# Performance work log

Measured on AMD Instinct MI355X. Metric: run time of the kernel, lower is better.

Reference implementation:

```python
import jax, jax.numpy as jnp
import numpy as np

N, K, C = 32768, 64, 256
PAIR, HID, BINS, CLIP = 32, 64, 16, 32
LN_EPS = 1e-5


def setup_inputs() -> dict:
    key = jax.random.key(0)
    ks = jax.random.split(key, 12)
    inp = {
        "features": jax.random.normal(ks[0], (N, C), jnp.float32),
        "resi": jnp.arange(N, dtype=jnp.int32),
        "chain": jax.random.randint(ks[1], (N,), 0, 4, jnp.int32),
        "batch": jax.random.randint(ks[2], (N,), 0, 8, jnp.int32),
        "neighbours": jax.random.randint(ks[3], (N, K), 0, N, jnp.int32),
        # learned params
        "W_left": jax.random.normal(ks[4], (C, PAIR), jnp.float32) / np.sqrt(C),
        "W_right": jax.random.normal(ks[5], (C, PAIR), jnp.float32) / np.sqrt(C),
        "W_pos": jax.random.normal(ks[6], (2 * CLIP + 1, PAIR), jnp.float32) * 0.1,
        "ln_scale": jnp.ones((PAIR,), jnp.float32),
        "ln_bias": jnp.zeros((PAIR,), jnp.float32),
        "W1": jax.random.normal(ks[7], (PAIR, HID), jnp.float32) / np.sqrt(PAIR),
        "b1": jnp.zeros((HID,), jnp.float32),
        "W2": jax.random.normal(ks[8], (HID, BINS), jnp.float32) / np.sqrt(HID),
        "b2": jnp.zeros((BINS,), jnp.float32),
    }
    return inp


def reference(features, resi, chain, batch, neighbours,
              W_left, W_right, W_pos, ln_scale, ln_bias, W1, b1, W2, b2):
    # left/right 32-dim codes, pairwise combine via neighbour gather: [N,K,32]
    left = features @ W_left
    right = features @ W_right
    dcode = left[:, None, :] + right[neighbours]

    # relative sequence position one-hot (65 classes) -> Linear(32, bias=False).
    # one_hot @ W_pos == row-gather of W_pos; masked to same chain & batch.
    rel = jnp.clip(resi[neighbours] - resi[:, None], -CLIP, CLIP) + CLIP  # [N,K]
    same = (chain[neighbours] == chain[:, None]) & (batch[neighbours] == batch[:, None])
    dcode = dcode + jnp.where(same[..., None], W_pos[rel], 0.0)

    # LayerNorm over last axis (scale + offset)
    mu = dcode.mean(-1, keepdims=True)
    var = jnp.mean(jnp.square(dcode - mu), -1, keepdims=True)
    dcode = (dcode - mu) * jax.lax.rsqrt(var + LN_EPS) * ln_scale + ln_bias

    # 2-layer GELU MLP -> 16 bins
    h = jax.nn.gelu(dcode @ W1 + b1)
    logits = h @ W2 + b2
    log_p = jax.nn.log_softmax(logits, axis=-1)

    # softmax-weighted expected distance over bin centers of [0, 22) A
    step = 22.0 / BINS
    bin_centers = (jnp.arange(BINS, dtype=jnp.float32) + 0.5) * step
    dmap = (jnp.exp(log_p) * bin_centers).sum(axis=-1)  # [N,K]
    return log_p, dmap
```

## Files before the change

### kernel.cpp

```cpp
#include <hip/hip_runtime.h>
#include <stdint.h>

#define N_RES 32768
#define KNEI  64
#define CFEAT 256
#define PAIRD 32
#define HIDD  64
#define NBINS 16
#define CLIPV 32
#define NGROUPS (N_RES * KNEI / 16)

typedef __attribute__((ext_vector_type(8))) short  short8;
typedef __attribute__((ext_vector_type(4))) float  float4_t;

union U8 { uint32_t u[4]; short8 s8; };

__device__ __forceinline__ uint32_t f2bf(float a, float b) {
    uint32_t ua = __float_as_uint(a);
    uint32_t ub = __float_as_uint(b);
    ua += 0x7fffu + ((ua >> 16) & 1u);
    ub += 0x7fffu + ((ub >> 16) & 1u);
    return (ua >> 16) | (ub & 0xffff0000u);
}

__device__ __forceinline__ float fastrcp(float x) { return __builtin_amdgcn_rcpf(x); }

__device__ __forceinline__ float gelu_tanh(float x) {
    float x2 = x * x;
    float inner = 0.7978845608028654f * x * (1.0f + 0.044715f * x2);
    float e = __expf(2.0f * inner);
    float th = 1.0f - 2.0f * fastrcp(e + 1.0f);
    return 0.5f * x * (1.0f + th);
}

__global__ __launch_bounds__(256) void proj_kernel(
    const float* __restrict__ feat, const float* __restrict__ Wl,
    const float* __restrict__ Wr, float* __restrict__ left,
    float* __restrict__ right)
{
    __shared__ __align__(16) float Wc[CFEAT * 64];
    const int tid = threadIdx.x;
    for (int idx = tid; idx < CFEAT * 32; idx += 256) {
        int i = idx >> 5, o = idx & 31;
        Wc[i * 64 + o]      = Wl[idx];
        Wc[i * 64 + 32 + o] = Wr[idx];
    }
    __syncthreads();

    const int cb   = (tid & 7) * 8;
    const int row0 = blockIdx.x * 128 + (tid >> 3) * 4;

    float acc[4][8];
#pragma unroll
    for (int r = 0; r < 4; ++r)
#pragma unroll
        for (int j = 0; j < 8; ++j) acc[r][j] = 0.f;

    for (int i = 0; i < CFEAT; i += 4) {
        float4_t f[4];
#pragma unroll
        for (int r = 0; r < 4; ++r)
            f[r] = *(const float4_t*)(feat + (size_t)(row0 + r) * CFEAT + i);
#pragma unroll
        for (int s = 0; s < 4; ++s) {
            float4_t wa = *(const float4_t*)(Wc + (i + s) * 64 + cb);
            float4_t wb = *(const float4_t*)(Wc + (i + s) * 64 + cb + 4);
#pragma unroll
            for (int r = 0; r < 4; ++r) {
                float fv = f[r][s];
#pragma unroll
                for (int j = 0; j < 4; ++j) {
                    acc[r][j]     += fv * wa[j];
                    acc[r][4 + j] += fv * wb[j];
                }
            }
        }
    }
#pragma unroll
    for (int r = 0; r < 4; ++r) {
        float* dst = (cb < 32) ? (left  + (size_t)(row0 + r) * 32 + cb)
                               : (right + (size_t)(row0 + r) * 32 + (cb - 32));
        float4_t v0 = {acc[r][0], acc[r][1], acc[r][2], acc[r][3]};
        float4_t v1 = {acc[r][4], acc[r][5], acc[r][6], acc[r][7]};
        *(float4_t*)dst       = v0;
        *(float4_t*)(dst + 4) = v1;
    }
}

__global__ __launch_bounds__(256) void pair_kernel(
    const float* __restrict__ left, const float* __restrict__ right,
    const int* __restrict__ resi, const int* __restrict__ chain,
    const int* __restrict__ batch, const int* __restrict__ nbr,
    const float* __restrict__ wpos, const float* __restrict__ lnS,
    const float* __restrict__ lnB, const float* __restrict__ W1,
    const float* __restrict__ b1, const float* __restrict__ W2,
    const float* __restrict__ b2, float* __restrict__ out_logp,
    float* __restrict__ out_dmap)
{
    __shared__ __align__(16) unsigned char Hbuf[4][16 * 144];

    const int tid    = threadIdx.x;
    const int lane   = tid & 63;
    const int wlocal = tid >> 6;
    const int q      = lane >> 4;
    const int c      = lane & 15;

    short8 w1a[4];
#pragma unroll
    for (int t = 0; t < 4; ++t) {
        U8 tmp;
#pragma unroll
        for (int v = 0; v < 4; ++v) {
            float a0 = W1[(q * 8 + 2 * v)     * HIDD + 16 * t + c];
            float a1 = W1[(q * 8 + 2 * v + 1) * HIDD + 16 * t + c];
            tmp.u[v] = f2bf(a0, a1);
        }
        w1a[t] = tmp.s8;
    }
    short8 w2a[2];
#pragma unroll
    for (int kt = 0; kt < 2; ++kt) {
        U8 tmp;
#pragma unroll
        for (int v = 0; v < 4; ++v) {
            float a0 = W2[(kt * 32 + q * 8 + 2 * v)     * NBINS + c];
            float a1 = W2[(kt * 32 + q * 8 + 2 * v + 1) * NBINS + c];
            tmp.u[v] = f2bf(a0, a1);
        }
        w2a[kt] = tmp.s8;
    }
    float4_t b1f[4];
#pragma unroll
    for (int t = 0; t < 4; ++t)
        b1f[t] = *(const float4_t*)(b1 + 16 * t + 4 * q);
    const float4_t b2f  = *(const float4_t*)(b2 + 4 * q);
    const float4_t lnS0 = *(const float4_t*)(lnS + 8 * q);
    const float4_t lnS1 = *(const float4_t*)(lnS + 8 * q + 4);
    const float4_t lnB0 = *(const float4_t*)(lnB + 8 * q);
    const float4_t lnB1 = *(const float4_t*)(lnB + 8 * q + 4);
    const float4_t zero4 = {0.f, 0.f, 0.f, 0.f};

    const int wglobal = (blockIdx.x * 256 + tid) >> 6;
    const int nwaves  = (gridDim.x * 256) >> 6;

    for (int g = wglobal; g < NGROUPS; g += nwaves) {
        const int pbase = g * 16;
        const int n = pbase >> 6;
        const int p = pbase + c;
        const int nb = nbr[p];
        const int rn = resi[n], cn = chain[n], bn = batch[n];
        int rel = resi[nb] - rn;
        rel = min(max(rel, -CLIPV), CLIPV) + CLIPV;
        const float msk = ((chain[nb] == cn) && (batch[nb] == bn)) ? 1.0f : 0.0f;

        const float* lptr = left  + (size_t)n  * PAIRD + 8 * q;
        const float* rptr = right + (size_t)nb * PAIRD + 8 * q;
        const float* pptr = wpos  + (size_t)rel * PAIRD + 8 * q;
        float4_t l0 = *(const float4_t*)lptr,       l1 = *(const float4_t*)(lptr + 4);
        float4_t r0 = *(const float4_t*)rptr,       r1 = *(const float4_t*)(rptr + 4);
        float4_t p0 = *(const float4_t*)pptr,       p1 = *(const float4_t*)(pptr + 4);
        float d[8];
#pragma unroll
        for (int j = 0; j < 4; ++j) {
            d[j]     = l0[j] + r0[j] + msk * p0[j];
            d[4 + j] = l1[j] + r1[j] + msk * p1[j];
        }

        float s1 = 0.f, s2 = 0.f;
#pragma unroll
        for (int j = 0; j < 8; ++j) { s1 += d[j]; s2 += d[j] * d[j]; }
        s1 += __shfl_xor(s1, 16, 64);  s1 += __shfl_xor(s1, 32, 64);
        s2 += __shfl_xor(s2, 16, 64);  s2 += __shfl_xor(s2, 32, 64);
        const float mu   = s1 * (1.0f / 32.0f);
        const float var  = s2 * (1.0f / 32.0f) - mu * mu;
        const float rstd = __builtin_amdgcn_rsqf(var + 1e-5f);

        U8 dpack;
#pragma unroll
        for (int v = 0; v < 4; ++v) {
            int j0 = 2 * v, j1 = 2 * v + 1;
            float sA = (j0 < 4) ? lnS0[j0 & 3] : lnS1[j0 & 3];
            float bA = (j0 < 4) ? lnB0[j0 & 3] : lnB1[j0 & 3];
            float sB = (j1 < 4) ? lnS0[j1 & 3] : lnS1[j1 & 3];
            float bB = (j1 < 4) ? lnB0[j1 & 3] : lnB1[j1 & 3];
            float nA = (d[j0] - mu) * rstd * sA + bA;
            float nB = (d[j1] - mu) * rstd * sB + bB;
            dpack.u[v] = f2bf(nA, nB);
        }
        const short8 dfrag = dpack.s8;

        float4_t hacc[4];
#pragma unroll
        for (int t = 0; t < 4; ++t)
            hacc[t] = __builtin_amdgcn_mfma_f32_16x16x32_bf16(w1a[t], dfrag, zero4, 0, 0, 0);

        unsigned char* hb = &Hbuf[wlocal][0] + c * 144;
#pragma unroll
        for (int t = 0; t < 4; ++t) {
            float g0 = gelu_tanh(hacc[t][0] + b1f[t][0]);
            float g1 = gelu_tanh(hacc[t][1] + b1f[t][1]);
            float g2 = gelu_tanh(hacc[t][2] + b1f[t][2]);
            float g3 = gelu_tanh(hacc[t][3] + b1f[t][3]);
            uint2 w; w.x = f2bf(g0, g1); w.y = f2bf(g2, g3);
            *(uint2*)(hb + 32 * t + 8 * q) = w;
        }
        __asm__ __volatile__("s_waitcnt lgkmcnt(0)" ::: "memory");
        const short8 hf0 = *(const short8*)(hb + 16 * q);
        const short8 hf1 = *(const short8*)(hb + 64 + 16 * q);

        float4_t lacc;
        lacc = __builtin_amdgcn_mfma_f32_16x16x32_bf16(w2a[0], hf0, zero4, 0, 0, 0);
        lacc = __builtin_amdgcn_mfma_f32_16x16x32_bf16(w2a[1], hf1, lacc,  0, 0, 0);

        float l[4];
#pragma unroll
        for (int r = 0; r < 4; ++r) l[r] = lacc[r] + b2f[r];

        float mx = fmaxf(fmaxf(l[0], l[1]), fmaxf(l[2], l[3]));
        mx = fmaxf(mx, __shfl_xor(mx, 16, 64));
        mx = fmaxf(mx, __shfl_xor(mx, 32, 64));
        float e[4];
#pragma unroll
        for (int r = 0; r < 4; ++r) e[r] = __expf(l[r] - mx);
        float ssum = (e[0] + e[1]) + (e[2] + e[3]);
        ssum += __shfl_xor(ssum, 16, 64);
        ssum += __shfl_xor(ssum, 32, 64);
        const float lse = __logf(ssum);

        float4_t lp = {l[0] - mx - lse, l[1] - mx - lse,
                       l[2] - mx - lse, l[3] - mx - lse};
        *(float4_t*)(out_logp + (size_t)p * NBINS + 4 * q) = lp;

        const float step  = 22.0f / NBINS;
        const float cbase = (4 * q + 0.5f) * step;
        float dpart = e[0] * cbase + e[1] * (cbase + step)
                    + e[2] * (cbase + 2 * step) + e[3] * (cbase + 3 * step);
        dpart += __shfl_xor(dpart, 16, 64);
        dpart += __shfl_xor(dpart, 32, 64);
        if (q == 0) out_dmap[p] = dpart * fastrcp(ssum);
    }
}

extern "C" void kernel_launch(void* const* d_in, const int* in_sizes, int n_in,
                              void* d_out, int out_size, void* d_ws, size_t ws_size,
                              hipStream_t stream) {
    const float* features = (const float*)d_in[0];
    const int*   resi     = (const int*)d_in[1];
    const int*   chain    = (const int*)d_in[2];
    const int*   batch    = (const int*)d_in[3];
    const int*   nbr      = (const int*)d_in[4];
    const float* W_left   = (const float*)d_in[5];
    const float* W_right  = (const float*)d_in[6];
    const float* W_pos    = (const float*)d_in[7];
    const float* ln_scale = (const float*)d_in[8];
    const float* ln_bias  = (const float*)d_in[9];
    const float* W1       = (const float*)d_in[10];
    const float* b1       = (const float*)d_in[11];
    const float* W2       = (const float*)d_in[12];
    const float* b2       = (const float*)d_in[13];

    float* left  = (float*)d_ws;
    float* right = left + (size_t)N_RES * PAIRD;

    float* out_logp = (float*)d_out;
    float* out_dmap = out_logp + (size_t)N_RES * KNEI * NBINS;

    proj_kernel<<<N_RES / 128, 256, 0, stream>>>(features, W_left, W_right, left, right);
    pair_kernel<<<2048, 256, 0, stream>>>(left, right, resi, chain, batch, nbr,
                                          W_pos, ln_scale, ln_bias, W1, b1, W2, b2,
                                          out_logp, out_dmap);
}
```

Measured before the change: 336.0 us.

## Fold LayerNorm affine into W1, drop softmax max, pack metadata, cheapen math

Folds the LayerNorm scale and bias into W1 and a precomputed b1 held in shared memory. The folded biases are fed as the MFMA accumulator input, and the softmax skips the max-subtraction and uses exp2/log2 intrinsics. GELU is rewritten around exp2 with folded constants, and bf16 packing uses an add-and-v_perm rounding instead of round-to-nearest-even. The projection kernel also writes a packed resi/chain/batch int4 array, so the pair kernel makes one gather per residue instead of three. The projection uses smaller row tiles, the pair kernel gains an occupancy hint, and an explicit LDS waitcnt is removed. Dropping the max subtraction risks overflow if logits get large, and the changed rounding shifts numerics slightly.

New measurement: 311.5 us. 7.3% less time.

```diff
diff --git a/kernel.cpp b/kernel.cpp
--- a/kernel.cpp
+++ b/kernel.cpp
@@ -15,71 +15,80 @@
 
 union U8 { uint32_t u[4]; short8 s8; };
 
-__device__ __forceinline__ uint32_t f2bf(float a, float b) {
-    uint32_t ua = __float_as_uint(a);
-    uint32_t ub = __float_as_uint(b);
-    ua += 0x7fffu + ((ua >> 16) & 1u);
-    ub += 0x7fffu + ((ub >> 16) & 1u);
-    return (ua >> 16) | (ub & 0xffff0000u);
+__device__ __forceinline__ uint32_t pkbf(float a, float b) {
+    uint32_t ua = __float_as_uint(a) + 0x8000u;
+    uint32_t ub = __float_as_uint(b) + 0x8000u;
+    uint32_t d;
+    const uint32_t sel = 0x07060302u;
+    asm("v_perm_b32 %0, %1, %2, %3" : "=v"(d) : "v"(ub), "v"(ua), "s"(sel));
+    return d;
 }
 
 __device__ __forceinline__ float fastrcp(float x) { return __builtin_amdgcn_rcpf(x); }
+__device__ __forceinline__ float fexp2(float x)   { return __builtin_amdgcn_exp2f(x); }
+__device__ __forceinline__ float flog2(float x)   { return __builtin_amdgcn_logf(x); }
 
 __device__ __forceinline__ float gelu_tanh(float x) {
+    const float k1 = 2.3022082f;
+    const float k2 = 0.1029432f;
     float x2 = x * x;
-    float inner = 0.7978845608028654f * x * (1.0f + 0.044715f * x2);
-    float e = __expf(2.0f * inner);
-    float th = 1.0f - 2.0f * fastrcp(e + 1.0f);
-    return 0.5f * x * (1.0f + th);
+    float t  = __builtin_fmaf(k2, x2, k1);
+    float e  = fexp2(x * t);
+    float th = __builtin_fmaf(-2.0f, fastrcp(e + 1.0f), 1.0f);
+    float hx = 0.5f * x;
+    return __builtin_fmaf(hx, th, hx);
 }
 
 __global__ __launch_bounds__(256) void proj_kernel(
     const float* __restrict__ feat, const float* __restrict__ Wl,
-    const float* __restrict__ Wr, float* __restrict__ left,
-    float* __restrict__ right)
+    const float* __restrict__ Wr, const int* __restrict__ resi,
+    const int* __restrict__ chain, const int* __restrict__ batch,
+    float* __restrict__ left, float* __restrict__ right,
+    int4* __restrict__ meta)
 {
     __shared__ __align__(16) float Wc[CFEAT * 64];
     const int tid = threadIdx.x;
     for (int idx = tid; idx < CFEAT * 32; idx += 256) {
-        int i = idx >> 5, o = idx & 31;
-        Wc[i * 64 + o]      = Wl[idx];
-        Wc[i * 64 + 32 + o] = Wr[idx];
+        int k = idx >> 5, o = idx & 31;
+        Wc[k * 64 + o]      = Wl[idx];
+        Wc[k * 64 + 32 + o] = Wr[idx];
+    }
+    const int row_base = blockIdx.x * 64;
+    if (meta != nullptr && tid < 64) {
+        int r = row_base + tid;
+        meta[r] = make_int4(resi[r], chain[r], batch[r], 0);
     }
     __syncthreads();
 
-    const int cb   = (tid & 7) * 8;
-    const int row0 = blockIdx.x * 128 + (tid >> 3) * 4;
-
-    float acc[4][8];
-#pragma unroll
-    for (int r = 0; r < 4; ++r)
+    const int cb = (tid & 7) * 8;
+    const int r0 = row_base + (tid >> 3) * 2;
+
+    float acc[2][8];
+#pragma unroll
+    for (int r = 0; r < 2; ++r)
 #pragma unroll
         for (int j = 0; j < 8; ++j) acc[r][j] = 0.f;
 
     for (int i = 0; i < CFEAT; i += 4) {
-        float4_t f[4];
-#pragma unroll
-        for (int r = 0; r < 4; ++r)
-            f[r] = *(const float4_t*)(feat + (size_t)(row0 + r) * CFEAT + i);
+        float4_t f0 = *(const float4_t*)(feat + (size_t)r0 * CFEAT + i);
+        float4_t f1 = *(const float4_t*)(feat + (size_t)(r0 + 1) * CFEAT + i);
 #pragma unroll
         for (int s = 0; s < 4; ++s) {
             float4_t wa = *(const float4_t*)(Wc + (i + s) * 64 + cb);
             float4_t wb = *(const float4_t*)(Wc + (i + s) * 64 + cb + 4);
 #pragma unroll
-            for (int r = 0; r < 4; ++r) {
-                float fv = f[r][s];
-#pragma unroll
-                for (int j = 0; j < 4; ++j) {
-                    acc[r][j]     += fv * wa[j];
-                    acc[r][4 + j] += fv * wb[j];
-                }
+            for (int j = 0; j < 4; ++j) {
+                acc[0][j]     += f0[s] * wa[j];
+                acc[0][4 + j] += f0[s] * wb[j];
+                acc[1][j]     += f1[s] * wa[j];
+                acc[1][4 + j] += f1[s] * wb[j];
             }
         }
     }
 #pragma unroll
-    for (int r = 0; r < 4; ++r) {
-        float* dst = (cb < 32) ? (left  + (size_t)(row0 + r) * 32 + cb)
-                               : (right + (size_t)(row0 + r) * 32 + (cb - 32));
+    for (int r = 0; r < 2; ++r) {
+        float* dst = (cb < 32) ? (left  + (size_t)(r0 + r) * 32 + cb)
+                               : (right + (size_t)(r0 + r) * 32 + (cb - 32));
         float4_t v0 = {acc[r][0], acc[r][1], acc[r][2], acc[r][3]};
         float4_t v1 = {acc[r][4], acc[r][5], acc[r][6], acc[r][7]};
         *(float4_t*)dst       = v0;
@@ -87,10 +96,12 @@
     }
 }
 
-__global__ __launch_bounds__(256) void pair_kernel(
+template <int USE_META>
+__global__ __launch_bounds__(256, 8) void pair_kernel(
     const float* __restrict__ left, const float* __restrict__ right,
     const int* __restrict__ resi, const int* __restrict__ chain,
     const int* __restrict__ batch, const int* __restrict__ nbr,
+    const int4* __restrict__ meta,
     const float* __restrict__ wpos, const float* __restrict__ lnS,
     const float* __restrict__ lnB, const float* __restrict__ W1,
     const float* __restrict__ b1, const float* __restrict__ W2,
@@ -98,6 +109,7 @@
     float* __restrict__ out_dmap)
 {
     __shared__ __align__(16) unsigned char Hbuf[4][16 * 144];
+    __shared__ __align__(16) float b1p[HIDD];
 
     const int tid    = threadIdx.x;
     const int lane   = tid & 63;
@@ -105,15 +117,23 @@
     const int q      = lane >> 4;
     const int c      = lane & 15;
 
+    if (tid < HIDD) {
+        float s = b1[tid];
+        for (int k = 0; k < PAIRD; ++k)
+            s = __builtin_fmaf(lnB[k], W1[k * HIDD + tid], s);
+        b1p[tid] = s;
+    }
+
     short8 w1a[4];
 #pragma unroll
     for (int t = 0; t < 4; ++t) {
         U8 tmp;
 #pragma unroll
         for (int v = 0; v < 4; ++v) {
-            float a0 = W1[(q * 8 + 2 * v)     * HIDD + 16 * t + c];
-            float a1 = W1[(q * 8 + 2 * v + 1) * HIDD + 16 * t + c];
-            tmp.u[v] = f2bf(a0, a1);
+            int k0 = q * 8 + 2 * v, k1 = k0 + 1;
+            float a0 = lnS[k0] * W1[k0 * HIDD + 16 * t + c];
+            float a1 = lnS[k1] * W1[k1 * HIDD + 16 * t + c];
+            tmp.u[v] = pkbf(a0, a1);
         }
         w1a[t] = tmp.s8;
     }
@@ -123,22 +143,14 @@
         U8 tmp;
 #pragma unroll
         for (int v = 0; v < 4; ++v) {
-            float a0 = W2[(kt * 32 + q * 8 + 2 * v)     * NBINS + c];
-            float a1 = W2[(kt * 32 + q * 8 + 2 * v + 1) * NBINS + c];
-            tmp.u[v] = f2bf(a0, a1);
+            int k0 = kt * 32 + q * 8 + 2 * v;
+            tmp.u[v] = pkbf(W2[k0 * NBINS + c], W2[(k0 + 1) * NBINS + c]);
         }
         w2a[kt] = tmp.s8;
     }
-    float4_t b1f[4];
-#pragma unroll
-    for (int t = 0; t < 4; ++t)
-        b1f[t] = *(const float4_t*)(b1 + 16 * t + 4 * q);
-    const float4_t b2f  = *(const float4_t*)(b2 + 4 * q);
-    const float4_t lnS0 = *(const float4_t*)(lnS + 8 * q);
-    const float4_t lnS1 = *(const float4_t*)(lnS + 8 * q + 4);
-    const float4_t lnB0 = *(const float4_t*)(lnB + 8 * q);
-    const float4_t lnB1 = *(const float4_t*)(lnB + 8 * q + 4);
-    const float4_t zero4 = {0.f, 0.f, 0.f, 0.f};
+    const float4_t b2f = *(const float4_t*)(b2 + 4 * q);
+
+    __syncthreads();
 
     const int wglobal = (blockIdx.x * 256 + tid) >> 6;
     const int nwaves  = (gridDim.x * 256) >> 6;
@@ -148,87 +160,84 @@
         const int n = pbase >> 6;
         const int p = pbase + c;
         const int nb = nbr[p];
-        const int rn = resi[n], cn = chain[n], bn = batch[n];
-        int rel = resi[nb] - rn;
-        rel = min(max(rel, -CLIPV), CLIPV) + CLIPV;
-        const float msk = ((chain[nb] == cn) && (batch[nb] == bn)) ? 1.0f : 0.0f;
+
+        int rel; float msk;
+        if (USE_META) {
+            int4 mn = meta[n];
+            int4 mb = meta[nb];
+            rel = min(max(mb.x - mn.x, -CLIPV), CLIPV) + CLIPV;
+            msk = ((mb.y == mn.y) && (mb.z == mn.z)) ? 1.0f : 0.0f;
+        } else {
+            rel = min(max(resi[nb] - resi[n], -CLIPV), CLIPV) + CLIPV;
+            msk = ((chain[nb] == chain[n]) && (batch[nb] == batch[n])) ? 1.0f : 0.0f;
+        }
 
         const float* lptr = left  + (size_t)n  * PAIRD + 8 * q;
         const float* rptr = right + (size_t)nb * PAIRD + 8 * q;
         const float* pptr = wpos  + (size_t)rel * PAIRD + 8 * q;
-        float4_t l0 = *(const float4_t*)lptr,       l1 = *(const float4_t*)(lptr + 4);
-        float4_t r0 = *(const float4_t*)rptr,       r1 = *(const float4_t*)(rptr + 4);
-        float4_t p0 = *(const float4_t*)pptr,       p1 = *(const float4_t*)(pptr + 4);
+        float4_t l0 = *(const float4_t*)lptr, l1 = *(const float4_t*)(lptr + 4);
+        float4_t r0 = *(const float4_t*)rptr, r1 = *(const float4_t*)(rptr + 4);
+        float4_t p0 = *(const float4_t*)pptr, p1 = *(const float4_t*)(pptr + 4);
         float d[8];
 #pragma unroll
         for (int j = 0; j < 4; ++j) {
-            d[j]     = l0[j] + r0[j] + msk * p0[j];
-            d[4 + j] = l1[j] + r1[j] + msk * p1[j];
+            d[j]     = __builtin_fmaf(msk, p0[j], l0[j] + r0[j]);
+            d[4 + j] = __builtin_fmaf(msk, p1[j], l1[j] + r1[j]);
         }
 
         float s1 = 0.f, s2 = 0.f;
 #pragma unroll
-        for (int j = 0; j < 8; ++j) { s1 += d[j]; s2 += d[j] * d[j]; }
+        for (int j = 0; j < 8; ++j) { s1 += d[j]; s2 = __builtin_fmaf(d[j], d[j], s2); }
         s1 += __shfl_xor(s1, 16, 64);  s1 += __shfl_xor(s1, 32, 64);
         s2 += __shfl_xor(s2, 16, 64);  s2 += __shfl_xor(s2, 32, 64);
         const float mu   = s1 * (1.0f / 32.0f);
-        const float var  = s2 * (1.0f / 32.0f) - mu * mu;
+        const float var  = __builtin_fmaf(-mu, mu, s2 * (1.0f / 32.0f));
         const float rstd = __builtin_amdgcn_rsqf(var + 1e-5f);
+        const float sh   = -mu * rstd;
 
         U8 dpack;
 #pragma unroll
         for (int v = 0; v < 4; ++v) {
-            int j0 = 2 * v, j1 = 2 * v + 1;
-            float sA = (j0 < 4) ? lnS0[j0 & 3] : lnS1[j0 & 3];
-            float bA = (j0 < 4) ? lnB0[j0 & 3] : lnB1[j0 & 3];
-            float sB = (j1 < 4) ? lnS0[j1 & 3] : lnS1[j1 & 3];
-            float bB = (j1 < 4) ? lnB0[j1 & 3] : lnB1[j1 & 3];
-            float nA = (d[j0] - mu) * rstd * sA + bA;
-            float nB = (d[j1] - mu) * rstd * sB + bB;
-            dpack.u[v] = f2bf(nA, nB);
+            float nA = __builtin_fmaf(d[2 * v],     rstd, sh);
+            float nB = __builtin_fmaf(d[2 * v + 1], rstd, sh);
+            dpack.u[v] = pkbf(nA, nB);
         }
         const short8 dfrag = dpack.s8;
 
         float4_t hacc[4];
 #pragma unroll
-        for (int t = 0; t < 4; ++t)
-            hacc[t] = __builtin_amdgcn_mfma_f32_16x16x32_bf16(w1a[t], dfrag, zero4, 0, 0, 0);
+        for (int t = 0; t < 4; ++t) {
+            float4_t c1 = *(const float4_t*)(b1p + 16 * t + 4 * q);
+            hacc[t] = __builtin_amdgcn_mfma_f32_16x16x32_bf16(w1a[t], dfrag, c1, 0, 0, 0);
+        }
 
         unsigned char* hb = &Hbuf[wlocal][0] + c * 144;
 #pragma unroll
         for (int t = 0; t < 4; ++t) {
-            float g0 = gelu_tanh(hacc[t][0] + b1f[t][0]);
-            float g1 = gelu_tanh(hacc[t][1] + b1f[t][1]);
-            float g2 = gelu_tanh(hacc[t][2] + b1f[t][2]);
-            float g3 = gelu_tanh(hacc[t][3] + b1f[t][3]);
-            uint2 w; w.x = f2bf(g0, g1); w.y = f2bf(g2, g3);
+            float g0 = gelu_tanh(hacc[t][0]);
+            float g1 = gelu_tanh(hacc[t][1]);
+            float g2 = gelu_tanh(hacc[t][2]);
+            float g3 = gelu_tanh(hacc[t][3]);
+            uint2 w; w.x = pkbf(g0, g1); w.y = pkbf(g2, g3);
             *(uint2*)(hb + 32 * t + 8 * q) = w;
         }
-        __asm__ __volatile__("s_waitcnt lgkmcnt(0)" ::: "memory");
         const short8 hf0 = *(const short8*)(hb + 16 * q);
         const short8 hf1 = *(const short8*)(hb + 64 + 16 * q);
 
         float4_t lacc;
-        lacc = __builtin_amdgcn_mfma_f32_16x16x32_bf16(w2a[0], hf0, zero4, 0, 0, 0);
-        lacc = __builtin_amdgcn_mfma_f32_16x16x32_bf16(w2a[1], hf1, lacc,  0, 0, 0);
-
-        float l[4];
-#pragma unroll
-        for (int r = 0; r < 4; ++r) l[r] = lacc[r] + b2f[r];
-
-        float mx = fmaxf(fmaxf(l[0], l[1]), fmaxf(l[2], l[3]));
-        mx = fmaxf(mx, __shfl_xor(mx, 16, 64));
-        mx = fmaxf(mx, __shfl_xor(mx, 32, 64));
+        lacc = __builtin_amdgcn_mfma_f32_16x16x32_bf16(w2a[0], hf0, b2f,  0, 0, 0);
+        lacc = __builtin_amdgcn_mfma_f32_16x16x32_bf16(w2a[1], hf1, lacc, 0, 0, 0);
+
+        const float LOG2E = 1.4426950408889634f, LN2 = 0.6931471805599453f;
         float e[4];
 #pragma unroll
-        for (int r = 0; r < 4; ++r) e[r] = __expf(l[r] - mx);
+        for (int r = 0; r < 4; ++r) e[r] = fexp2(lacc[r] * LOG2E);
         float ssum = (e[0] + e[1]) + (e[2] + e[3]);
         ssum += __shfl_xor(ssum, 16, 64);
         ssum += __shfl_xor(ssum, 32, 64);
-        const float lse = __logf(ssum);
-
-        float4_t lp = {l[0] - mx - lse, l[1] - mx - lse,
-                       l[2] - mx - lse, l[3] - mx - lse};
+        const float lse = flog2(ssum) * LN2;
+
+        float4_t lp = {lacc[0] - lse, lacc[1] - lse, lacc[2] - lse, lacc[3] - lse};
         *(float4_t*)(out_logp + (size_t)p * NBINS + 4 * q) = lp;
 
         const float step  = 22.0f / NBINS;
@@ -261,12 +270,22 @@
 
     float* left  = (float*)d_ws;
     float* right = left + (size_t)N_RES * PAIRD;
+    const size_t base_bytes = (size_t)2 * N_RES * PAIRD * sizeof(float);
+    const size_t meta_bytes = (size_t)N_RES * sizeof(int4);
+    const bool use_meta = ws_size >= base_bytes + meta_bytes;
+    int4* meta = use_meta ? (int4*)((char*)d_ws + base_bytes) : nullptr;
 
     float* out_logp = (float*)d_out;
     float* out_dmap = out_logp + (size_t)N_RES * KNEI * NBINS;
 
-    proj_kernel<<<N_RES / 128, 256, 0, stream>>>(features, W_left, W_right, left, right);
-    pair_kernel<<<2048, 256, 0, stream>>>(left, right, resi, chain, batch, nbr,
-                                          W_pos, ln_scale, ln_bias, W1, b1, W2, b2,
-                                          out_logp, out_dmap);
-}
+    proj_kernel<<<N_RES / 64, 256, 0, stream>>>(features, W_left, W_right,
+                                                resi, chain, batch, left, right, meta);
+    if (use_meta)
+        pair_kernel<1><<<2048, 256, 0, stream>>>(left, right, resi, chain, batch, nbr,
+                                                 meta, W_pos, ln_scale, ln_bias, W1, b1,
+                                                 W2, b2, out_logp, out_dmap);
+    else
+        pair_kernel<0><<<2048, 256, 0, stream>>>(left, right, resi, chain, batch, nbr,
+                                                 nullptr, W_pos, ln_scale, ln_bias, W1, b1,
+                                                 W2, b2, out_logp, out_dmap);
+}
```
